# Kernel tuning notes

Hardware: AMD Instinct MI355X
Metric: run time of the kernel (lower is better)

The kernel has to match this reference:

```python
import jax, jax.numpy as jnp
import numpy as np

N = 100000      # nodes
E = 1000000     # edges per relation
D_IN = 128
D_OUT = 128
SLOPE = 0.2
N_REL = 3


def setup_inputs() -> dict:
    key = jax.random.key(0)
    ks = jax.random.split(key, 1 + 4 * N_REL)
    inp = {"H": jax.random.normal(ks[0], (N, D_IN), dtype=jnp.float32)}
    xav_w = float(np.sqrt(6.0 / (D_IN + D_OUT)))   # xavier_uniform bound for W
    xav_a = float(np.sqrt(6.0 / (1 + 2 * D_OUT)))  # xavier_uniform on a viewed as [1, 2d]
    for i in range(N_REL):
        inp[f"row_{i}"] = jax.random.randint(ks[1 + 4 * i], (E,), 0, N, dtype=jnp.int64)
        inp[f"col_{i}"] = jax.random.randint(ks[2 + 4 * i], (E,), 0, N, dtype=jnp.int64)
        inp[f"W_{i}"] = jax.random.uniform(ks[3 + 4 * i], (D_IN, D_OUT), jnp.float32, -xav_w, xav_w)
        inp[f"a_{i}"] = jax.random.uniform(ks[4 + 4 * i], (2 * D_OUT,), jnp.float32, -xav_a, xav_a)
    inp["bias"] = jnp.zeros((D_OUT,), jnp.float32)
    return inp


def _relation_agg(H, W, a, row, col):
    # 1) transform: Wh = H @ W_r  [N, d]
    Wh = H @ W
    d = Wh.shape[1]
    # 2) edge scores: e_ij = leaky_relu(a[:d].Wh[row] + a[d:].Wh[col])
    s_dst = Wh @ a[:d]   # coefficient for destination (row) side  [N]
    s_src = Wh @ a[d:]   # coefficient for source (col) side       [N]
    e = jax.nn.leaky_relu(s_dst[row] + s_src[col], negative_slope=SLOPE)  # [E]
    # 3) segment softmax over incoming edges of each destination node
    e_max = jax.ops.segment_max(e, row, num_segments=N)          # [N]
    e_shift = jnp.exp(e - e_max[row])                            # [E]
    e_sum = jax.ops.segment_sum(e_shift, row, num_segments=N)    # [N]
    alpha = e_shift / jnp.maximum(e_sum[row], 1e-12)             # [E]
    # 4) weighted aggregation of source features
    return jax.ops.segment_sum(alpha[:, None] * Wh[col], row, num_segments=N)  # [N, d]


def reference(H, row_0, col_0, row_1, col_1, row_2, col_2,
              W_0, W_1, W_2, a_0, a_1, a_2, bias):
    rows = (row_0, row_1, row_2)
    cols = (col_0, col_1, col_2)
    Ws = (W_0, W_1, W_2)
    As = (a_0, a_1, a_2)
    agg = jnp.zeros((N, D_OUT), H.dtype)
    for r in range(N_REL):
        agg = agg + _relation_agg(H, Ws[r], As[r], rows[r], cols[r])
    return agg + bias
```

## Files before the change

kernel.cpp:

```cpp
#include <hip/hip_runtime.h>

#define SLOPE 0.2f

typedef unsigned int uint;
typedef unsigned short ushort;
typedef __attribute__((ext_vector_type(8))) short short8;
typedef __attribute__((ext_vector_type(4))) float f32x4;

#define BINW 2048
#define BINSHIFT 11

__device__ inline ushort f2bf(float f) {
    uint u = __float_as_uint(f);
    uint r = (u + 0x7FFFu + ((u >> 16) & 1u)) >> 16;
    return (ushort)r;
}
__device__ inline uint pack2bf(float lo, float hi) {
    return (uint)f2bf(lo) | ((uint)f2bf(hi) << 16);
}
__device__ inline float bfl(uint u) { return __uint_as_float(u << 16); }
__device__ inline float bfh(uint u) { return __uint_as_float(u & 0xFFFF0000u); }

__global__ void wt3(const float* __restrict__ W0, const float* __restrict__ W1,
                    const float* __restrict__ W2, ushort* __restrict__ WT) {
    int r = blockIdx.x;
    const float* W = (r == 0) ? W0 : (r == 1) ? W1 : W2;
    ushort* wt = WT + r * 16384;
    for (int i = threadIdx.x; i < 16384; i += 256) {
        int k = i >> 7, n = i & 127;
        wt[n * 128 + k] = f2bf(W[i]);
    }
}

__global__ __launch_bounds__(256) void gemm3(const float* __restrict__ H,
                                             const ushort* __restrict__ WT,
                                             const float* __restrict__ a0,
                                             const float* __restrict__ a1,
                                             const float* __restrict__ a2,
                                             ushort* __restrict__ Wh0,
                                             ushort* __restrict__ Wh1,
                                             ushort* __restrict__ Wh2,
                                             float* __restrict__ sd,
                                             float* __restrict__ ss, int N) {
    __shared__ ushort lds[16384];
    __shared__ float sds[128], sss[128];
    const int brow = blockIdx.x * 128;
    const int t = threadIdx.x;

    for (int c = t; c < 2048; c += 256) {
        int r = c >> 4;
        int kb = (c & 15) << 4;
        int gr = brow + r;
        uint4 u = make_uint4(0, 0, 0, 0);
        if (gr < N) {
            const float* hp = H + (size_t)gr * 128 + (kb >> 1);
            float4 v0 = *reinterpret_cast<const float4*>(hp);
            float4 v1 = *reinterpret_cast<const float4*>(hp + 4);
            u.x = pack2bf(v0.x, v0.y);
            u.y = pack2bf(v0.z, v0.w);
            u.z = pack2bf(v1.x, v1.y);
            u.w = pack2bf(v1.z, v1.w);
        }
        int dst = (r << 8) + (kb ^ ((r & 7) << 4));
        *reinterpret_cast<uint4*>((char*)lds + dst) = u;
    }
    if (t < 128) { sds[t] = 0.f; sss[t] = 0.f; }
    __syncthreads();

    const int wave = t >> 6, lane = t & 63;
    const int l16 = lane & 15, lhi = lane >> 4;

    for (int rel = 0; rel < 3; ++rel) {
        ushort* Wh = (rel == 0) ? Wh0 : (rel == 1) ? Wh1 : Wh2;
        const float* aP = (rel == 0) ? a0 : (rel == 1) ? a1 : a2;
        const ushort* wt = WT + rel * 16384;

        short8 bf[2][4];
#pragma unroll
        for (int nt = 0; nt < 2; ++nt) {
            int n = wave * 32 + nt * 16 + l16;
#pragma unroll
            for (int ks = 0; ks < 4; ++ks)
                bf[nt][ks] = *reinterpret_cast<const short8*>(wt + n * 128 + ks * 32 + lhi * 8);
        }

        f32x4 acc[8][2];
#pragma unroll
        for (int mt = 0; mt < 8; ++mt) { acc[mt][0] = (f32x4)(0.f); acc[mt][1] = (f32x4)(0.f); }

#pragma unroll
        for (int ks = 0; ks < 4; ++ks) {
#pragma unroll
            for (int mt = 0; mt < 8; ++mt) {
                int r = mt * 16 + l16;
                int kb = (ks * 32 + lhi * 8) * 2;
                int addr = (r << 8) + (kb ^ ((r & 7) << 4));
                short8 af = *reinterpret_cast<const short8*>((char*)lds + addr);
                acc[mt][0] = __builtin_amdgcn_mfma_f32_16x16x32_bf16(af, bf[0][ks], acc[mt][0], 0, 0, 0);
                acc[mt][1] = __builtin_amdgcn_mfma_f32_16x16x32_bf16(af, bf[1][ks], acc[mt][1], 0, 0, 0);
            }
        }

        const int c0 = wave * 32 + l16;
        const float aL0 = aP[c0], aL1 = aP[c0 + 16];
        const float aR0 = aP[128 + c0], aR1 = aP[128 + c0 + 16];
#pragma unroll
        for (int mt = 0; mt < 8; ++mt)
#pragma unroll
            for (int reg = 0; reg < 4; ++reg) {
                float pd = acc[mt][0][reg] * aL0 + acc[mt][1][reg] * aL1;
                float ps = acc[mt][0][reg] * aR0 + acc[mt][1][reg] * aR1;
#pragma unroll
                for (int off = 1; off < 16; off <<= 1) {
                    pd += __shfl_xor(pd, off);
                    ps += __shfl_xor(ps, off);
                }
                if (l16 == 0) {
                    int rloc = mt * 16 + lhi * 4 + reg;
                    atomicAdd(&sds[rloc], pd);
                    atomicAdd(&sss[rloc], ps);
                }
            }

#pragma unroll
        for (int mt = 0; mt < 8; ++mt)
#pragma unroll
            for (int nt = 0; nt < 2; ++nt)
#pragma unroll
                for (int reg = 0; reg < 4; ++reg) {
                    int gr = brow + mt * 16 + lhi * 4 + reg;
                    if (gr < N)
                        Wh[(size_t)gr * 128 + wave * 32 + nt * 16 + l16] = f2bf(acc[mt][nt][reg]);
                }

        __syncthreads();
        if (t < 128) {
            int gr = brow + t;
            if (gr < N) { sd[rel * N + gr] = sds[t]; ss[rel * N + gr] = sss[t]; }
            sds[t] = 0.f; sss[t] = 0.f;
        }
        __syncthreads();
    }
}

__global__ __launch_bounds__(256) void binhist(const int* __restrict__ r0,
                                               const int* __restrict__ r1,
                                               const int* __restrict__ r2,
                                               int* __restrict__ bincnt, int E, int N, int nbins) {
    __shared__ int h[256];
    int t = threadIdx.x;
    h[t] = 0;
    __syncthreads();
    int base = blockIdx.x * 4096;
#pragma unroll
    for (int k = 0; k < 16; ++k) {
        int i = base + k * 256 + t;
        if (i < 3 * E) {
            int r = (i >= 2 * E) ? 2 : (i >= E) ? 1 : 0;
            int li = i - r * E;
            const int* rp = (r == 0) ? r0 : (r == 1) ? r1 : r2;
            int idx = r * N + __builtin_nontemporal_load(rp + li);
            atomicAdd(&h[idx >> BINSHIFT], 1);
        }
    }
    __syncthreads();
    if (t < nbins && h[t]) atomicAdd(&bincnt[t], h[t]);
}

__global__ __launch_bounds__(256) void binscan(const int* __restrict__ bincnt,
                                               int* __restrict__ binbase,
                                               int* __restrict__ gbincur, int nbins, int total) {
    __shared__ int sA[256], sB[256];
    int t = threadIdx.x;
    int v = (t < nbins) ? bincnt[t] : 0;
    sA[t] = v;
    __syncthreads();
    int* pa = sA; int* pb = sB;
    for (int off = 1; off < 256; off <<= 1) {
        int x = pa[t] + ((t >= off) ? pa[t - off] : 0);
        pb[t] = x;
        __syncthreads();
        int* tmp = pa; pa = pb; pb = tmp;
    }
    if (t < nbins) {
        int excl = pa[t] - v;
        binbase[t] = excl;
        gbincur[t] = excl;
    }
    if (t == 0) binbase[nbins] = total;
}

__global__ __launch_bounds__(256) void binscatter(const int* __restrict__ r0, const int* __restrict__ r1,
                                                  const int* __restrict__ r2, const int* __restrict__ c0,
                                                  const int* __restrict__ c1, const int* __restrict__ c2,
                                                  const float* __restrict__ sd, const float* __restrict__ ss,
                                                  int* __restrict__ gbincur, uint2* __restrict__ binned,
                                                  int E, int N, int nbins) {
    __shared__ uint2 staged[4096];
    __shared__ int hist[256], sB[256], curi[256], gbase[256];
    const int t = threadIdx.x;
    hist[t] = 0;
    __syncthreads();

    uint2 rec[16];
    short bn[16];
    const int base = blockIdx.x * 4096;
#pragma unroll
    for (int k = 0; k < 16; ++k) {
        int i = base + k * 256 + t;
        bn[k] = -1;
        if (i < 3 * E) {
            int r = (i >= 2 * E) ? 2 : (i >= E) ? 1 : 0;
            int li = i - r * E;
            const int* rp = (r == 0) ? r0 : (r == 1) ? r1 : r2;
            const int* cp = (r == 0) ? c0 : (r == 1) ? c1 : c2;
            int rr = __builtin_nontemporal_load(rp + li);
            int cc = __builtin_nontemporal_load(cp + li);
            int idx = r * N + rr;
            int b = idx >> BINSHIFT;
            uint lo = (uint)(idx & (BINW - 1));
            float x = sd[idx] + ss[r * N + cc];
            x = (x > 0.f) ? x : SLOPE * x;
            float w = __expf(x);
            rec[k] = make_uint2((uint)cc | (lo << 17), __float_as_uint(w));
            bn[k] = (short)b;
            atomicAdd(&hist[b], 1);
        }
    }
    __syncthreads();

    int v = hist[t];
    int* pa = hist; int* pb = sB;
    for (int off = 1; off < 256; off <<= 1) {
        int x = pa[t] + ((t >= off) ? pa[t - off] : 0);
        pb[t] = x;
        __syncthreads();
        int* tmp = pa; pa = pb; pb = tmp;
    }
    sB[t] = pa[t] - v;
    curi[t] = pa[t] - v;
    if (t < nbins && v > 0) gbase[t] = atomicAdd(&gbincur[t], v);
    __syncthreads();

#pragma unroll
    for (int k = 0; k < 16; ++k)
        if (bn[k] >= 0) {
            int p = atomicAdd(&curi[bn[k]], 1);
            staged[p] = rec[k];
        }
    __syncthreads();

    const int wave = t >> 6, lane = t & 63;
    for (int b = wave; b < nbins; b += 4) {
        int s = sB[b];
        int len = hist[b] - s;
        if (len <= 0) continue;
        int g = gbase[b];
        for (int j = lane; j < len; j += 64) binned[g + j] = staged[s + j];
    }
}

__global__ __launch_bounds__(256) void binsort(const uint2* __restrict__ binned,
                                               const int* __restrict__ binbase,
                                               uint2* __restrict__ wc, int* __restrict__ offs, int L) {
    __shared__ int s1[BINW];
    __shared__ int wsum[4];
    const int b = blockIdx.x, t = threadIdx.x;
    const int start = binbase[b], end = binbase[b + 1];
    const int ibase = b << BINSHIFT;
    const int width = min(BINW, L - ibase);

    for (int i = t; i < BINW; i += 256) s1[i] = 0;
    __syncthreads();
    for (int j = start + t; j < end; j += 256)
        atomicAdd(&s1[(binned[j].x >> 17) & (BINW - 1)], 1);
    __syncthreads();

    const int cb = t * 8;
    int v[8];
    int run = 0;
#pragma unroll
    for (int k = 0; k < 8; ++k) { run += s1[cb + k]; v[k] = run; }
    const int lane = t & 63, wv = t >> 6;
    int x = run;
#pragma unroll
    for (int off = 1; off < 64; off <<= 1) {
        int y = __shfl_up(x, off);
        if (lane >= off) x += y;
    }
    if (lane == 63) wsum[wv] = x;
    __syncthreads();
    int pre = x - run;
#pragma unroll
    for (int w = 0; w < 3; ++w) if (wv > w) pre += wsum[w];

#pragma unroll
    for (int k = 0; k < 8; ++k) {
        int i = cb + k;
        if (i < width) offs[ibase + i] = start + pre + v[k];
    }
#pragma unroll
    for (int k = 0; k < 8; ++k)
        s1[cb + k] = start + pre + (k ? v[k - 1] : 0);
    __syncthreads();

    for (int j = start + t; j < end; j += 256) {
        uint2 r = binned[j];
        uint lo = (r.x >> 17) & (BINW - 1);
        int p = atomicAdd(&s1[lo], 1);
        wc[p] = make_uint2(r.y, r.x & 0x1FFFFu);
    }
}

__global__ __launch_bounds__(256) void aggregate3(const uint* __restrict__ wh0,
                                                  const uint* __restrict__ wh1,
                                                  const uint* __restrict__ wh2,
                                                  const uint2* __restrict__ wc,
                                                  const int* __restrict__ offs,
                                                  const float* __restrict__ bias,
                                                  float* __restrict__ out, int N) {
    int node = blockIdx.x * 16 + (threadIdx.x >> 4);
    int ql = threadIdx.x & 15;
    if (node >= N) return;

    float t0 = 0.f, t1 = 0.f, t2 = 0.f, t3 = 0.f, t4 = 0.f, t5 = 0.f, t6 = 0.f, t7 = 0.f;

#pragma unroll
    for (int r = 0; r < 3; ++r) {
        const uint* wh = (r == 0) ? wh0 : (r == 1) ? wh1 : wh2;
        int idx = r * N + node;
        int end = offs[idx];
        int beg = (idx == 0) ? 0 : offs[idx - 1];
        if (beg >= end) continue;
        float wsum = 0.f;
        float a0 = 0.f, a1 = 0.f, a2 = 0.f, a3 = 0.f, a4 = 0.f, a5 = 0.f, a6 = 0.f, a7 = 0.f;
        for (int j = beg; j < end; ++j) {
            uint2 e = wc[j];
            float w = __uint_as_float(e.x);
            int c = (int)e.y;
            uint4 v = reinterpret_cast<const uint4*>(wh + ((size_t)c << 6))[ql];
            wsum += w;
            a0 = fmaf(w, bfl(v.x), a0);
            a1 = fmaf(w, bfh(v.x), a1);
            a2 = fmaf(w, bfl(v.y), a2);
            a3 = fmaf(w, bfh(v.y), a3);
            a4 = fmaf(w, bfl(v.z), a4);
            a5 = fmaf(w, bfh(v.z), a5);
            a6 = fmaf(w, bfl(v.w), a6);
            a7 = fmaf(w, bfh(v.w), a7);
        }
        float inv = 1.f / fmaxf(wsum, 1e-12f);
        t0 = fmaf(a0, inv, t0); t1 = fmaf(a1, inv, t1);
        t2 = fmaf(a2, inv, t2); t3 = fmaf(a3, inv, t3);
        t4 = fmaf(a4, inv, t4); t5 = fmaf(a5, inv, t5);
        t6 = fmaf(a6, inv, t6); t7 = fmaf(a7, inv, t7);
    }

    float4 b0 = *reinterpret_cast<const float4*>(bias + ql * 8);
    float4 b1 = *reinterpret_cast<const float4*>(bias + ql * 8 + 4);
    float* o = out + (size_t)node * 128 + ql * 8;
    f32x4 o0 = {t0 + b0.x, t1 + b0.y, t2 + b0.z, t3 + b0.w};
    f32x4 o1 = {t4 + b1.x, t5 + b1.y, t6 + b1.z, t7 + b1.w};
    __builtin_nontemporal_store(o0, reinterpret_cast<f32x4*>(o));
    __builtin_nontemporal_store(o1, reinterpret_cast<f32x4*>(o + 4));
}

extern "C" void kernel_launch(void* const* d_in, const int* in_sizes, int n_in,
                              void* d_out, int out_size, void* d_ws, size_t ws_size,
                              hipStream_t stream) {
    const float* H = (const float*)d_in[0];
    const int* row[3] = {(const int*)d_in[1], (const int*)d_in[5], (const int*)d_in[9]};
    const int* col[3] = {(const int*)d_in[2], (const int*)d_in[6], (const int*)d_in[10]};
    const float* W[3] = {(const float*)d_in[3], (const float*)d_in[7], (const float*)d_in[11]};
    const float* a[3] = {(const float*)d_in[4], (const float*)d_in[8], (const float*)d_in[12]};
    const float* bias = (const float*)d_in[13];

    const int N = in_sizes[0] / 128;
    const int E = in_sizes[1];
    float* out = (float*)d_out;

    const int L = 3 * N;
    const int nbins = (L + BINW - 1) >> BINSHIFT;

    char* ws = (char*)d_ws;
    size_t off = 0;
    auto alloc = [&](size_t bytes) -> void* {
        void* p = ws + off;
        off += (bytes + 255) & ~(size_t)255;
        return p;
    };

    ushort* WT = (ushort*)alloc(3 * 16384 * 2);
    ushort* Wh[3];
    for (int r = 0; r < 3; ++r) Wh[r] = (ushort*)alloc((size_t)N * 128 * 2);
    float* sd = (float*)alloc((size_t)L * 4);
    float* ss = (float*)alloc((size_t)L * 4);
    int* offs = (int*)alloc((size_t)L * 4);
    int* bincnt = (int*)alloc((size_t)(nbins + 2) * 4);
    int* binbase = (int*)alloc((size_t)(nbins + 2) * 4);
    int* gbincur = (int*)alloc((size_t)(nbins + 2) * 4);
    uint2* wc = (uint2*)alloc((size_t)3 * E * 8);
    uint2* binned = (uint2*)d_out;

    const int nbG = (N + 127) / 128;
    const int nbQ = (N + 15) / 16;
    const int nbB = (3 * E + 4095) / 4096;

    wt3<<<3, 256, 0, stream>>>(W[0], W[1], W[2], WT);
    gemm3<<<nbG, 256, 0, stream>>>(H, WT, a[0], a[1], a[2], Wh[0], Wh[1], Wh[2], sd, ss, N);

    hipMemsetAsync(bincnt, 0, (size_t)(nbins + 2) * 4, stream);
    binhist<<<nbB, 256, 0, stream>>>(row[0], row[1], row[2], bincnt, E, N, nbins);
    binscan<<<1, 256, 0, stream>>>(bincnt, binbase, gbincur, nbins, 3 * E);
    binscatter<<<nbB, 256, 0, stream>>>(row[0], row[1], row[2], col[0], col[1], col[2],
                                        sd, ss, gbincur, binned, E, N, nbins);
    binsort<<<nbins, 256, 0, stream>>>(binned, binbase, wc, offs, L);

    aggregate3<<<nbQ, 256, 0, stream>>>((const uint*)Wh[0], (const uint*)Wh[1], (const uint*)Wh[2],
                                        wc, offs, bias, out, N);
}
```

Baseline: 354.0 us.

## Split score computation out of GEMM and unroll aggregation gather loop by four

Removes the per-row attention score reductions (shuffles, LDS atomics, extra barriers) from the GEMM epilogue and computes them in a separate kernel that rereads the bf16 Wh rows. Scores now come from bf16-rounded Wh instead of fp32 accumulators, which slightly changes numerics. The aggregation loop is unrolled by four with two independent accumulator sets so more gathers are in flight per thread. The cost is an extra kernel launch and an extra read of all three Wh arrays.

New measurement: 319.0 us. 9.9% less time.

```diff
diff --git a/kernel.cpp b/kernel.cpp
--- a/kernel.cpp
+++ b/kernel.cpp
@@ -34,16 +34,10 @@
 
 __global__ __launch_bounds__(256) void gemm3(const float* __restrict__ H,
                                              const ushort* __restrict__ WT,
-                                             const float* __restrict__ a0,
-                                             const float* __restrict__ a1,
-                                             const float* __restrict__ a2,
                                              ushort* __restrict__ Wh0,
                                              ushort* __restrict__ Wh1,
-                                             ushort* __restrict__ Wh2,
-                                             float* __restrict__ sd,
-                                             float* __restrict__ ss, int N) {
+                                             ushort* __restrict__ Wh2, int N) {
     __shared__ ushort lds[16384];
-    __shared__ float sds[128], sss[128];
     const int brow = blockIdx.x * 128;
     const int t = threadIdx.x;
 
@@ -64,7 +58,6 @@
         int dst = (r << 8) + (kb ^ ((r & 7) << 4));
         *reinterpret_cast<uint4*>((char*)lds + dst) = u;
     }
-    if (t < 128) { sds[t] = 0.f; sss[t] = 0.f; }
     __syncthreads();
 
     const int wave = t >> 6, lane = t & 63;
@@ -72,7 +65,6 @@
 
     for (int rel = 0; rel < 3; ++rel) {
         ushort* Wh = (rel == 0) ? Wh0 : (rel == 1) ? Wh1 : Wh2;
-        const float* aP = (rel == 0) ? a0 : (rel == 1) ? a1 : a2;
         const ushort* wt = WT + rel * 16384;
 
         short8 bf[2][4];
@@ -101,27 +93,6 @@
             }
         }
 
-        const int c0 = wave * 32 + l16;
-        const float aL0 = aP[c0], aL1 = aP[c0 + 16];
-        const float aR0 = aP[128 + c0], aR1 = aP[128 + c0 + 16];
-#pragma unroll
-        for (int mt = 0; mt < 8; ++mt)
-#pragma unroll
-            for (int reg = 0; reg < 4; ++reg) {
-                float pd = acc[mt][0][reg] * aL0 + acc[mt][1][reg] * aL1;
-                float ps = acc[mt][0][reg] * aR0 + acc[mt][1][reg] * aR1;
-#pragma unroll
-                for (int off = 1; off < 16; off <<= 1) {
-                    pd += __shfl_xor(pd, off);
-                    ps += __shfl_xor(ps, off);
-                }
-                if (l16 == 0) {
-                    int rloc = mt * 16 + lhi * 4 + reg;
-                    atomicAdd(&sds[rloc], pd);
-                    atomicAdd(&sss[rloc], ps);
-                }
-            }
-
 #pragma unroll
         for (int mt = 0; mt < 8; ++mt)
 #pragma unroll
@@ -132,14 +103,41 @@
                     if (gr < N)
                         Wh[(size_t)gr * 128 + wave * 32 + nt * 16 + l16] = f2bf(acc[mt][nt][reg]);
                 }
-
-        __syncthreads();
-        if (t < 128) {
-            int gr = brow + t;
-            if (gr < N) { sd[rel * N + gr] = sds[t]; ss[rel * N + gr] = sss[t]; }
-            sds[t] = 0.f; sss[t] = 0.f;
-        }
-        __syncthreads();
+    }
+}
+
+__global__ __launch_bounds__(256) void scores_k(const uint* __restrict__ wh0,
+                                                const uint* __restrict__ wh1,
+                                                const uint* __restrict__ wh2,
+                                                const float* __restrict__ a0,
+                                                const float* __restrict__ a1,
+                                                const float* __restrict__ a2,
+                                                float* __restrict__ sd,
+                                                float* __restrict__ ss, int N) {
+    int node = blockIdx.x * 16 + (threadIdx.x >> 4);
+    int ql = threadIdx.x & 15;
+    if (node >= N) return;
+#pragma unroll
+    for (int r = 0; r < 3; ++r) {
+        const uint* wh = (r == 0) ? wh0 : (r == 1) ? wh1 : wh2;
+        const float* a = (r == 0) ? a0 : (r == 1) ? a1 : a2;
+        const uint4 v = reinterpret_cast<const uint4*>(wh + ((size_t)node << 6))[ql];
+        float f0 = bfl(v.x), f1 = bfh(v.x), f2 = bfl(v.y), f3 = bfh(v.y);
+        float f4 = bfl(v.z), f5 = bfh(v.z), f6 = bfl(v.w), f7 = bfh(v.w);
+        float4 aL0 = *reinterpret_cast<const float4*>(a + ql * 8);
+        float4 aL1 = *reinterpret_cast<const float4*>(a + ql * 8 + 4);
+        float4 aR0 = *reinterpret_cast<const float4*>(a + 128 + ql * 8);
+        float4 aR1 = *reinterpret_cast<const float4*>(a + 128 + ql * 8 + 4);
+        float pd = f0 * aL0.x + f1 * aL0.y + f2 * aL0.z + f3 * aL0.w +
+                   f4 * aL1.x + f5 * aL1.y + f6 * aL1.z + f7 * aL1.w;
+        float ps = f0 * aR0.x + f1 * aR0.y + f2 * aR0.z + f3 * aR0.w +
+                   f4 * aR1.x + f5 * aR1.y + f6 * aR1.z + f7 * aR1.w;
+#pragma unroll
+        for (int off = 1; off < 16; off <<= 1) {
+            pd += __shfl_xor(pd, off);
+            ps += __shfl_xor(ps, off);
+        }
+        if (ql == 0) { sd[r * N + node] = pd; ss[r * N + node] = ps; }
     }
 }
 
@@ -332,28 +330,54 @@
         int end = offs[idx];
         int beg = (idx == 0) ? 0 : offs[idx - 1];
         if (beg >= end) continue;
-        float wsum = 0.f;
+
+        float wsA = 0.f, wsB = 0.f;
         float a0 = 0.f, a1 = 0.f, a2 = 0.f, a3 = 0.f, a4 = 0.f, a5 = 0.f, a6 = 0.f, a7 = 0.f;
-        for (int j = beg; j < end; ++j) {
+        float g0 = 0.f, g1 = 0.f, g2 = 0.f, g3 = 0.f, g4 = 0.f, g5 = 0.f, g6 = 0.f, g7 = 0.f;
+
+        int j = beg;
+        for (; j + 4 <= end; j += 4) {
+            uint2 e0 = wc[j], e1 = wc[j + 1], e2 = wc[j + 2], e3 = wc[j + 3];
+            uint4 v0 = reinterpret_cast<const uint4*>(wh + ((size_t)e0.y << 6))[ql];
+            uint4 v1 = reinterpret_cast<const uint4*>(wh + ((size_t)e1.y << 6))[ql];
+            uint4 v2 = reinterpret_cast<const uint4*>(wh + ((size_t)e2.y << 6))[ql];
+            uint4 v3 = reinterpret_cast<const uint4*>(wh + ((size_t)e3.y << 6))[ql];
+            float w0 = __uint_as_float(e0.x), w1 = __uint_as_float(e1.x);
+            float w2 = __uint_as_float(e2.x), w3 = __uint_as_float(e3.x);
+            wsA += w0 + w2;
+            wsB += w1 + w3;
+            a0 = fmaf(w0, bfl(v0.x), a0); a1 = fmaf(w0, bfh(v0.x), a1);
+            a2 = fmaf(w0, bfl(v0.y), a2); a3 = fmaf(w0, bfh(v0.y), a3);
+            a4 = fmaf(w0, bfl(v0.z), a4); a5 = fmaf(w0, bfh(v0.z), a5);
+            a6 = fmaf(w0, bfl(v0.w), a6); a7 = fmaf(w0, bfh(v0.w), a7);
+            g0 = fmaf(w1, bfl(v1.x), g0); g1 = fmaf(w1, bfh(v1.x), g1);
+            g2 = fmaf(w1, bfl(v1.y), g2); g3 = fmaf(w1, bfh(v1.y), g3);
+            g4 = fmaf(w1, bfl(v1.z), g4); g5 = fmaf(w1, bfh(v1.z), g5);
+            g6 = fmaf(w1, bfl(v1.w), g6); g7 = fmaf(w1, bfh(v1.w), g7);
+            a0 = fmaf(w2, bfl(v2.x), a0); a1 = fmaf(w2, bfh(v2.x), a1);
+            a2 = fmaf(w2, bfl(v2.y), a2); a3 = fmaf(w2, bfh(v2.y), a3);
+            a4 = fmaf(w2, bfl(v2.z), a4); a5 = fmaf(w2, bfh(v2.z), a5);
+            a6 = fmaf(w2, bfl(v2.w), a6); a7 = fmaf(w2, bfh(v2.w), a7);
+            g0 = fmaf(w3, bfl(v3.x), g0); g1 = fmaf(w3, bfh(v3.x), g1);
+            g2 = fmaf(w3, bfl(v3.y), g2); g3 = fmaf(w3, bfh(v3.y), g3);
+            g4 = fmaf(w3, bfl(v3.z), g4); g5 = fmaf(w3, bfh(v3.z), g5);
+            g6 = fmaf(w3, bfl(v3.w), g6); g7 = fmaf(w3, bfh(v3.w), g7);
+        }
+        for (; j < end; ++j) {
             uint2 e = wc[j];
             float w = __uint_as_float(e.x);
-            int c = (int)e.y;
-            uint4 v = reinterpret_cast<const uint4*>(wh + ((size_t)c << 6))[ql];
-            wsum += w;
-            a0 = fmaf(w, bfl(v.x), a0);
-            a1 = fmaf(w, bfh(v.x), a1);
-            a2 = fmaf(w, bfl(v.y), a2);
-            a3 = fmaf(w, bfh(v.y), a3);
-            a4 = fmaf(w, bfl(v.z), a4);
-            a5 = fmaf(w, bfh(v.z), a5);
-            a6 = fmaf(w, bfl(v.w), a6);
-            a7 = fmaf(w, bfh(v.w), a7);
-        }
-        float inv = 1.f / fmaxf(wsum, 1e-12f);
-        t0 = fmaf(a0, inv, t0); t1 = fmaf(a1, inv, t1);
-        t2 = fmaf(a2, inv, t2); t3 = fmaf(a3, inv, t3);
-        t4 = fmaf(a4, inv, t4); t5 = fmaf(a5, inv, t5);
-        t6 = fmaf(a6, inv, t6); t7 = fmaf(a7, inv, t7);
+            uint4 v = reinterpret_cast<const uint4*>(wh + ((size_t)e.y << 6))[ql];
+            wsA += w;
+            a0 = fmaf(w, bfl(v.x), a0); a1 = fmaf(w, bfh(v.x), a1);
+            a2 = fmaf(w, bfl(v.y), a2); a3 = fmaf(w, bfh(v.y), a3);
+            a4 = fmaf(w, bfl(v.z), a4); a5 = fmaf(w, bfh(v.z), a5);
+            a6 = fmaf(w, bfl(v.w), a6); a7 = fmaf(w, bfh(v.w), a7);
+        }
+        float inv = 1.f / fmaxf(wsA + wsB, 1e-12f);
+        t0 = fmaf(a0 + g0, inv, t0); t1 = fmaf(a1 + g1, inv, t1);
+        t2 = fmaf(a2 + g2, inv, t2); t3 = fmaf(a3 + g3, inv, t3);
+        t4 = fmaf(a4 + g4, inv, t4); t5 = fmaf(a5 + g5, inv, t5);
+        t6 = fmaf(a6 + g6, inv, t6); t7 = fmaf(a7 + g7, inv, t7);
     }
 
     float4 b0 = *reinterpret_cast<const float4*>(bias + ql * 8);
@@ -407,7 +431,9 @@
     const int nbB = (3 * E + 4095) / 4096;
 
     wt3<<<3, 256, 0, stream>>>(W[0], W[1], W[2], WT);
-    gemm3<<<nbG, 256, 0, stream>>>(H, WT, a[0], a[1], a[2], Wh[0], Wh[1], Wh[2], sd, ss, N);
+    gemm3<<<nbG, 256, 0, stream>>>(H, WT, Wh[0], Wh[1], Wh[2], N);
+    scores_k<<<nbQ, 256, 0, stream>>>((const uint*)Wh[0], (const uint*)Wh[1], (const uint*)Wh[2],
+                                      a[0], a[1], a[2], sd, ss, N);
 
     hipMemsetAsync(bincnt, 0, (size_t)(nbins + 2) * 4, stream);
     binhist<<<nbB, 256, 0, stream>>>(row[0], row[1], row[2], bincnt, E, N, nbins);
```
